# Optimization experiments

Measured on AMD Instinct MI355X. Metric: run time of the kernel, lower is better.

The kernel has to match this reference:

```python
import jax, jax.numpy as jnp
import numpy as np

B = 128
K = 16
# (in_ch, featdim, dim) per stage, matching conv1..conv11
DIMS = [(3, 8, 2048), (8, 32, 1024), (32, 64, 512), (64, 64, 256), (64, 64, 128),
        (64, 128, 64), (128, 256, 32), (256, 512, 16), (512, 512, 8), (512, 512, 4),
        (512, 1024, 2)]


def setup_inputs() -> dict:
    key = jax.random.key(0)
    ks = jax.random.split(key, 64)
    inp = {"x": jax.random.normal(ks[0], (B, 3, 2048), dtype=jnp.float32)}
    i = 1
    for li, (cin, cf, d) in enumerate(DIMS, start=1):
        inp[f"W{li}"] = jax.random.normal(ks[i], (3 * cf, cin), dtype=jnp.float32) / np.sqrt(cin).astype(np.float32); i += 1
        inp[f"b{li}"] = jax.random.normal(ks[i], (3 * cf,), dtype=jnp.float32) * 0.01; i += 1
        inp[f"sel{li}"] = jax.random.randint(ks[i], (d,), 0, 3); i += 1
    inp["fcW"] = jax.random.normal(ks[i], (K, 1024), dtype=jnp.float32) / np.sqrt(1024).astype(np.float32); i += 1
    inp["fcb"] = jax.random.normal(ks[i], (K,), dtype=jnp.float32) * 0.01
    return inp


def kdconv(x, W, b, sel, featdim, dim):
    # 1x1 conv == per-position matmul: x [B, Cin, dim] -> y [B, 3*featdim, dim]
    y = jax.nn.relu(jnp.einsum('oi,bin->bon', W, x) + b[None, :, None])
    y = y.reshape(-1, featdim, 3, dim)
    # kd split-dim gather: pick one of the 3 feature groups per position
    y = jnp.take_along_axis(y, sel[None, None, None, :], axis=2)[:, :, 0, :]  # [B, featdim, dim]
    # pairwise max-pool of sibling leaves
    return y.reshape(-1, featdim, dim // 2, 2).max(axis=-1)  # [B, featdim, dim//2]


def reference(x, sel1, sel2, sel3, sel4, sel5, sel6, sel7, sel8, sel9, sel10, sel11,
              W1, b1, W2, b2, W3, b3, W4, b4, W5, b5, W6, b6, W7, b7, W8, b8,
              W9, b9, W10, b10, W11, b11, fcW, fcb):
    Ws = [W1, W2, W3, W4, W5, W6, W7, W8, W9, W10, W11]
    bs = [b1, b2, b3, b4, b5, b6, b7, b8, b9, b10, b11]
    sels = [sel1, sel2, sel3, sel4, sel5, sel6, sel7, sel8, sel9, sel10, sel11]
    h = x
    for (cin, cf, d), W, b, s in zip(DIMS, Ws, bs, sels):
        h = kdconv(h, W, b, s, cf, d)
    h = h.reshape(-1, 1024)  # [B, 1024]
    return jax.nn.log_softmax(h @ fcW.T + fcb, axis=-1)
```

## Files before the change

kernel.cpp:

```cpp
#include <hip/hip_runtime.h>
#include <math.h>

typedef __attribute__((ext_vector_type(8))) short bf16x8;
typedef __attribute__((ext_vector_type(4))) float f32x4;

__device__ __forceinline__ unsigned short f2bf(float f) {
    unsigned u = __builtin_bit_cast(unsigned, f);
    u += 0x7FFF + ((u >> 16) & 1);
    return (unsigned short)(u >> 16);
}
__device__ __forceinline__ float bf2f(unsigned short h) {
    unsigned u = ((unsigned)h) << 16;
    return __builtin_bit_cast(float, u);
}

struct K1Params {
    const float* x;
    const float* W1; const float* B1; const int* S1;
    const float* W2; const float* B2; const int* S2;
    const float* Wsrc[9];
    unsigned short* Wb;
    unsigned short* X3;
};

__global__ __launch_bounds__(256) void k1_kernel(K1Params P)
{
    const int tid = threadIdx.x;

    if (blockIdx.x >= 128) {
        int gt = (blockIdx.x - 128) * 256 + tid;
        const int we[9] = {6144, 12288, 12288, 24576, 98304, 393216, 786432, 786432, 1572864};
        int off = 0;
#pragma unroll
        for (int li = 0; li < 9; ++li) {
            const float4* src = (const float4*)P.Wsrc[li];
            ushort4* dst = (ushort4*)(P.Wb + off);
            int n4 = we[li] >> 2;
            for (int i = gt; i < n4; i += 32768) {
                float4 w = src[i];
                dst[i] = make_ushort4(f2bf(w.x), f2bf(w.y), f2bf(w.z), f2bf(w.w));
            }
            off += we[li];
        }
        return;
    }

    __shared__ float wl1[72], bl1[24], wl2[768], bl2[96];
    __shared__ unsigned short bufL1[16 * 64 * 8];

    if (tid < 72) wl1[tid] = P.W1[tid];
    if (tid >= 128 && tid < 152) bl1[tid - 128] = P.B1[tid - 128];
    for (int i = tid; i < 768; i += 256) wl2[i] = P.W2[i];
    if (tid < 96) bl2[tid] = P.B2[tid];
    __syncthreads();

    const int npT = blockIdx.x >> 1;
    const int b0  = (blockIdx.x & 1) * 64;

    for (int i = tid; i < 1024; i += 256) {
        int pos_l = i >> 6, bl = i & 63;
        int np1 = npT * 16 + pos_l;
        int b = b0 + bl;
        int s0 = P.S1[2 * np1], s1 = P.S1[2 * np1 + 1];
        const float* xb = P.x + (size_t)b * 6144 + 2 * np1;
        float2 c0 = *(const float2*)(xb);
        float2 c1 = *(const float2*)(xb + 2048);
        float2 c2 = *(const float2*)(xb + 4096);
        unsigned short o[8];
#pragma unroll
        for (int f = 0; f < 8; ++f) {
            int r0 = f * 3 + s0, r1 = f * 3 + s1;
            float z0 = fmaf(wl1[r0*3+2], c2.x, fmaf(wl1[r0*3+1], c1.x, fmaf(wl1[r0*3+0], c0.x, bl1[r0])));
            float z1 = fmaf(wl1[r1*3+2], c2.y, fmaf(wl1[r1*3+1], c1.y, fmaf(wl1[r1*3+0], c0.y, bl1[r1])));
            o[f] = f2bf(fmaxf(fmaxf(z0, z1), 0.f));
        }
        unsigned short* dst = &bufL1[((size_t)pos_l * 64 + bl) * 8];
        *(ushort4*)dst       = make_ushort4(o[0], o[1], o[2], o[3]);
        *(ushort4*)(dst + 4) = make_ushort4(o[4], o[5], o[6], o[7]);
    }
    __syncthreads();

    for (int i = tid; i < 512; i += 256) {
        int np_l = i >> 6, bl = i & 63;
        int np2 = npT * 8 + np_l;
        int s0 = P.S2[2 * np2], s1 = P.S2[2 * np2 + 1];
        const unsigned short* r0 = &bufL1[((size_t)(2 * np_l) * 64 + bl) * 8];
        const unsigned short* r1 = &bufL1[((size_t)(2 * np_l + 1) * 64 + bl) * 8];
        float xa[8], xb[8];
        {
            ushort4 u0 = *(const ushort4*)r0, u1 = *(const ushort4*)(r0 + 4);
            ushort4 v0 = *(const ushort4*)r1, v1 = *(const ushort4*)(r1 + 4);
            xa[0]=bf2f(u0.x); xa[1]=bf2f(u0.y); xa[2]=bf2f(u0.z); xa[3]=bf2f(u0.w);
            xa[4]=bf2f(u1.x); xa[5]=bf2f(u1.y); xa[6]=bf2f(u1.z); xa[7]=bf2f(u1.w);
            xb[0]=bf2f(v0.x); xb[1]=bf2f(v0.y); xb[2]=bf2f(v0.z); xb[3]=bf2f(v0.w);
            xb[4]=bf2f(v1.x); xb[5]=bf2f(v1.y); xb[6]=bf2f(v1.z); xb[7]=bf2f(v1.w);
        }
        unsigned short o[32];
#pragma unroll
        for (int f = 0; f < 32; ++f) {
            const float* w0 = &wl2[(f * 3 + s0) * 8];
            const float* w1 = &wl2[(f * 3 + s1) * 8];
            float z0 = bl2[f * 3 + s0], z1 = bl2[f * 3 + s1];
#pragma unroll
            for (int k = 0; k < 8; ++k) {
                z0 = fmaf(w0[k], xa[k], z0);
                z1 = fmaf(w1[k], xb[k], z1);
            }
            o[f] = f2bf(fmaxf(fmaxf(z0, z1), 0.f));
        }
        unsigned short* dst = P.X3 + ((size_t)np2 * 128 + b0 + bl) * 32;
#pragma unroll
        for (int i2 = 0; i2 < 8; ++i2)
            *(ushort4*)(dst + 4 * i2) = make_ushort4(o[4*i2], o[4*i2+1], o[4*i2+2], o[4*i2+3]);
    }
}

template<int CIN>
__device__ __forceinline__ void mfma_tile(
    const unsigned short* a0, const unsigned short* a1,
    const unsigned short* b0p, const unsigned short* b1p,
    f32x4& acc0, f32x4& acc1)
{
#pragma unroll
    for (int k = 0; k < CIN; k += 32) {
        bf16x8 A0 = __builtin_bit_cast(bf16x8, *(const float4*)(const void*)(a0 + k));
        bf16x8 A1 = __builtin_bit_cast(bf16x8, *(const float4*)(const void*)(a1 + k));
        bf16x8 B0 = __builtin_bit_cast(bf16x8, *(const float4*)(const void*)(b0p + k));
        bf16x8 B1 = __builtin_bit_cast(bf16x8, *(const float4*)(const void*)(b1p + k));
        acc0 = __builtin_amdgcn_mfma_f32_16x16x32_bf16(A0, B0, acc0, 0, 0, 0);
        acc1 = __builtin_amdgcn_mfma_f32_16x16x32_bf16(A1, B1, acc1, 0, 0, 0);
    }
}

__device__ __forceinline__ void epilogue_store(
    unsigned short* dst, const f32x4& acc0, const f32x4& acc1,
    const float* bias, int fbase, int s0, int s1)
{
    unsigned short o[4];
#pragma unroll
    for (int r = 0; r < 4; ++r) {
        float v = fmaxf(fmaxf(acc0[r] + bias[(fbase + r) * 3 + s0],
                              acc1[r] + bias[(fbase + r) * 3 + s1]), 0.f);
        o[r] = f2bf(v);
    }
    *(ushort4*)dst = make_ushort4(o[0], o[1], o[2], o[3]);
}

__global__ __launch_bounds__(256) void stage2_kernel(
    const unsigned short* __restrict__ X3,
    const unsigned short* __restrict__ Wb,
    const float* __restrict__ B3, const int* __restrict__ S3,
    const float* __restrict__ B4, const int* __restrict__ S4,
    const float* __restrict__ B5, const int* __restrict__ S5,
    unsigned short* __restrict__ X6)
{
    constexpr int RPE = 72;
    __shared__ unsigned short L3o[4 * 32 * RPE];
    __shared__ unsigned short L4o[2 * 32 * RPE];

    const int tid  = threadIdx.x;
    const int lane = tid & 63;
    const int wv   = tid >> 6;
    const int c = lane & 15, q = lane >> 4;
    const int n5 = blockIdx.x >> 2;
    const int b0 = (blockIdx.x & 3) * 32;

    const unsigned short* W3b = Wb;
    const unsigned short* W4b = Wb + 6144;
    const unsigned short* W5b = Wb + 18432;

    for (int t = wv; t < 32; t += 4) {
        int bt = t & 1, ft = (t >> 1) & 3, j = t >> 3;
        int np = 4 * n5 + j;
        int s0 = __builtin_amdgcn_readfirstlane(S3[2 * np]);
        int s1 = __builtin_amdgcn_readfirstlane(S3[2 * np + 1]);
        int f0 = ft * 16, bl = bt * 16;
        const unsigned short* a0 = W3b + (size_t)((f0 + c) * 3 + s0) * 32 + q * 8;
        const unsigned short* a1 = W3b + (size_t)((f0 + c) * 3 + s1) * 32 + q * 8;
        const unsigned short* bp0 = X3 + ((size_t)(8 * n5 + 2 * j) * 128 + b0 + bl + c) * 32 + q * 8;
        const unsigned short* bp1 = X3 + ((size_t)(8 * n5 + 2 * j + 1) * 128 + b0 + bl + c) * 32 + q * 8;
        f32x4 acc0 = {0.f,0.f,0.f,0.f}, acc1 = {0.f,0.f,0.f,0.f};
        mfma_tile<32>(a0, a1, bp0, bp1, acc0, acc1);
        epilogue_store(&L3o[((size_t)j * 32 + bl + c) * RPE + f0 + q * 4],
                       acc0, acc1, B3, f0 + q * 4, s0, s1);
    }
    __syncthreads();

    for (int t = wv; t < 16; t += 4) {
        int bt = t & 1, ft = (t >> 1) & 3, j = t >> 3;
        int np = 2 * n5 + j;
        int s0 = __builtin_amdgcn_readfirstlane(S4[2 * np]);
        int s1 = __builtin_amdgcn_readfirstlane(S4[2 * np + 1]);
        int f0 = ft * 16, bl = bt * 16;
        const unsigned short* a0 = W4b + (size_t)((f0 + c) * 3 + s0) * 64 + q * 8;
        const unsigned short* a1 = W4b + (size_t)((f0 + c) * 3 + s1) * 64 + q * 8;
        const unsigned short* bp0 = &L3o[((size_t)(2 * j) * 32 + bl + c) * RPE + q * 8];
        const unsigned short* bp1 = &L3o[((size_t)(2 * j + 1) * 32 + bl + c) * RPE + q * 8];
        f32x4 acc0 = {0.f,0.f,0.f,0.f}, acc1 = {0.f,0.f,0.f,0.f};
        mfma_tile<64>(a0, a1, bp0, bp1, acc0, acc1);
        epilogue_store(&L4o[((size_t)j * 32 + bl + c) * RPE + f0 + q * 4],
                       acc0, acc1, B4, f0 + q * 4, s0, s1);
    }
    __syncthreads();

    for (int t = wv; t < 8; t += 4) {
        int bt = t & 1, ft = t >> 1;
        int s0 = __builtin_amdgcn_readfirstlane(S5[2 * n5]);
        int s1 = __builtin_amdgcn_readfirstlane(S5[2 * n5 + 1]);
        int f0 = ft * 16, bl = bt * 16;
        const unsigned short* a0 = W5b + (size_t)((f0 + c) * 3 + s0) * 64 + q * 8;
        const unsigned short* a1 = W5b + (size_t)((f0 + c) * 3 + s1) * 64 + q * 8;
        const unsigned short* bp0 = &L4o[((size_t)(0) * 32 + bl + c) * RPE + q * 8];
        const unsigned short* bp1 = &L4o[((size_t)(1) * 32 + bl + c) * RPE + q * 8];
        f32x4 acc0 = {0.f,0.f,0.f,0.f}, acc1 = {0.f,0.f,0.f,0.f};
        mfma_tile<64>(a0, a1, bp0, bp1, acc0, acc1);
        epilogue_store(X6 + ((size_t)n5 * 128 + b0 + bl + c) * 64 + f0 + q * 4,
                       acc0, acc1, B5, f0 + q * 4, s0, s1);
    }
}

__global__ __launch_bounds__(512) void stage67_kernel(
    const unsigned short* __restrict__ X6,
    const unsigned short* __restrict__ W6b, const float* __restrict__ B6, const int* __restrict__ S6,
    const unsigned short* __restrict__ W7b, const float* __restrict__ B7, const int* __restrict__ S7,
    unsigned short* __restrict__ X8)
{
    constexpr int RPE = 136;
    __shared__ unsigned short L6o[2 * 16 * RPE];

    const int tid  = threadIdx.x;
    const int lane = tid & 63;
    const int wv   = tid >> 6;
    const int c = lane & 15, q = lane >> 4;
    const int n7 = blockIdx.x >> 3;
    const int b0 = (blockIdx.x & 7) * 16;

    for (int t = wv; t < 16; t += 8) {
        int j = t >> 3, ft = t & 7;
        int np = 2 * n7 + j;
        int s0 = __builtin_amdgcn_readfirstlane(S6[2 * np]);
        int s1 = __builtin_amdgcn_readfirstlane(S6[2 * np + 1]);
        int f0 = ft * 16;
        const unsigned short* a0 = W6b + (size_t)((f0 + c) * 3 + s0) * 64 + q * 8;
        const unsigned short* a1 = W6b + (size_t)((f0 + c) * 3 + s1) * 64 + q * 8;
        const unsigned short* bp0 = X6 + ((size_t)(2 * np) * 128 + b0 + c) * 64 + q * 8;
        const unsigned short* bp1 = X6 + ((size_t)(2 * np + 1) * 128 + b0 + c) * 64 + q * 8;
        f32x4 acc0 = {0.f,0.f,0.f,0.f}, acc1 = {0.f,0.f,0.f,0.f};
        mfma_tile<64>(a0, a1, bp0, bp1, acc0, acc1);
        epilogue_store(&L6o[((size_t)j * 16 + c) * RPE + f0 + q * 4],
                       acc0, acc1, B6, f0 + q * 4, s0, s1);
    }
    __syncthreads();

    {
        int s0 = __builtin_amdgcn_readfirstlane(S7[2 * n7]);
        int s1 = __builtin_amdgcn_readfirstlane(S7[2 * n7 + 1]);
        for (int t = wv; t < 16; t += 8) {
            int f0 = t * 16;
            const unsigned short* a0 = W7b + (size_t)((f0 + c) * 3 + s0) * 128 + q * 8;
            const unsigned short* a1 = W7b + (size_t)((f0 + c) * 3 + s1) * 128 + q * 8;
            const unsigned short* bp0 = &L6o[((size_t)(0) * 16 + c) * RPE + q * 8];
            const unsigned short* bp1 = &L6o[((size_t)(1) * 16 + c) * RPE + q * 8];
            f32x4 acc0 = {0.f,0.f,0.f,0.f}, acc1 = {0.f,0.f,0.f,0.f};
            mfma_tile<128>(a0, a1, bp0, bp1, acc0, acc1);
            epilogue_store(X8 + ((size_t)n7 * 128 + b0 + c) * 256 + f0 + q * 4,
                           acc0, acc1, B7, f0 + q * 4, s0, s1);
        }
    }
}

template<int CIN, int CF, int NP, int MW, int NW>
__global__ __launch_bounds__(256) void mfma_kernel(
    const unsigned short* __restrict__ Xin,
    const unsigned short* __restrict__ Wb,
    const float* __restrict__ bias,
    const int*   __restrict__ sel,
    unsigned short* __restrict__ Xout)
{
    constexpr int FT = CF / (16 * MW);
    constexpr int BT = 128 / (16 * NW);

    const int wid  = threadIdx.x >> 6;
    const int lane = threadIdx.x & 63;
    const int task = blockIdx.x * 4 + wid;
    const int bi = task % BT;
    const int fi = (task / BT) % FT;
    const int n  = task / (BT * FT);

    const int c = lane & 15;
    const int q = lane >> 4;
    const int s0 = __builtin_amdgcn_readfirstlane(sel[2 * n]);
    const int s1 = __builtin_amdgcn_readfirstlane(sel[2 * n + 1]);

    const int f0 = fi * 16 * MW;
    const int b0 = bi * 16 * NW;

    const unsigned short* ap[2][MW];
    const unsigned short* bp[2][NW];
#pragma unroll
    for (int p = 0; p < 2; ++p) {
        int s = p ? s1 : s0;
#pragma unroll
        for (int mi = 0; mi < MW; ++mi)
            ap[p][mi] = Wb + (size_t)((f0 + mi * 16 + c) * 3 + s) * CIN + q * 8;
#pragma unroll
        for (int ni = 0; ni < NW; ++ni)
            bp[p][ni] = Xin + ((size_t)(2 * n + p) * 128 + b0 + ni * 16 + c) * CIN + q * 8;
    }

    f32x4 acc[2][MW][NW];
#pragma unroll
    for (int p = 0; p < 2; ++p)
#pragma unroll
        for (int mi = 0; mi < MW; ++mi)
#pragma unroll
            for (int ni = 0; ni < NW; ++ni)
                acc[p][mi][ni] = (f32x4){0.f, 0.f, 0.f, 0.f};

#pragma unroll 2
    for (int k = 0; k < CIN; k += 32) {
        bf16x8 A[2][MW], B[2][NW];
#pragma unroll
        for (int p = 0; p < 2; ++p) {
#pragma unroll
            for (int mi = 0; mi < MW; ++mi)
                A[p][mi] = __builtin_bit_cast(bf16x8, *(const float4*)(const void*)(ap[p][mi] + k));
#pragma unroll
            for (int ni = 0; ni < NW; ++ni)
                B[p][ni] = __builtin_bit_cast(bf16x8, *(const float4*)(const void*)(bp[p][ni] + k));
        }
#pragma unroll
        for (int p = 0; p < 2; ++p)
#pragma unroll
            for (int mi = 0; mi < MW; ++mi)
#pragma unroll
                for (int ni = 0; ni < NW; ++ni)
                    acc[p][mi][ni] = __builtin_amdgcn_mfma_f32_16x16x32_bf16(
                        A[p][mi], B[p][ni], acc[p][mi][ni], 0, 0, 0);
    }

#pragma unroll
    for (int mi = 0; mi < MW; ++mi) {
        int fbase = f0 + mi * 16 + q * 4;
#pragma unroll
        for (int ni = 0; ni < NW; ++ni) {
            int b = b0 + ni * 16 + c;
            epilogue_store(Xout + ((size_t)n * 128 + b) * CF + fbase,
                           acc[0][mi][ni], acc[1][mi][ni], bias, fbase, s0, s1);
        }
    }
}

__global__ __launch_bounds__(256) void fc_logsoftmax_kernel(
    const unsigned short* __restrict__ h, const float* __restrict__ fcW,
    const float* __restrict__ fcb, float* __restrict__ out)
{
    int b   = blockIdx.x;
    int tid = threadIdx.x;
    int k     = tid & 15;
    int chunk = tid >> 4;

    const float* __restrict__ wk = fcW + (size_t)k * 1024;
    const unsigned short* hb = h + (size_t)b * 1024;

    float partial = 0.0f;
    int j0 = chunk * 64;
#pragma unroll 8
    for (int j = 0; j < 64; ++j)
        partial = fmaf(bf2f(hb[j0 + j]), wk[j0 + j], partial);

    __shared__ float red[16][17];
    red[chunk][k] = partial;
    __syncthreads();

    __shared__ float logits[16];
    if (tid < 16) {
        float s = fcb[tid];
#pragma unroll
        for (int c = 0; c < 16; ++c) s += red[c][tid];
        logits[tid] = s;
    }
    __syncthreads();

    if (tid < 16) {
        float mx = -INFINITY;
#pragma unroll
        for (int kk = 0; kk < 16; ++kk) mx = fmaxf(mx, logits[kk]);
        float se = 0.0f;
#pragma unroll
        for (int kk = 0; kk < 16; ++kk) se += expf(logits[kk] - mx);
        out[b * 16 + tid] = logits[tid] - mx - logf(se);
    }
}

extern "C" void kernel_launch(void* const* d_in, const int* in_sizes, int n_in,
                              void* d_out, int out_size, void* d_ws, size_t ws_size,
                              hipStream_t stream)
{
#define WL(i) (const float*)d_in[1 + 3 * (i)]
#define BL(i) (const float*)d_in[2 + 3 * (i)]
#define SL(i) (const int*)  d_in[3 + 3 * (i)]

    unsigned short* bufA = (unsigned short*)d_ws;
    unsigned short* bufB = bufA + 2u * 1024u * 1024u;
    unsigned short* Wb   = bufB + 2u * 1024u * 1024u;

    const int o6 = 30720, o7 = 55296, o8 = 153600,
              o9 = 546816, o10 = 1333248, o11 = 2119680;

    K1Params P;
    P.x = (const float*)d_in[0];
    P.W1 = WL(0); P.B1 = BL(0); P.S1 = SL(0);
    P.W2 = WL(1); P.B2 = BL(1); P.S2 = SL(1);
    for (int i = 0; i < 9; ++i) P.Wsrc[i] = WL(2 + i);
    P.Wb = Wb; P.X3 = bufA;
    k1_kernel<<<256, 256, 0, stream>>>(P);

    stage2_kernel<<<256, 256, 0, stream>>>(bufA, Wb,
        BL(2), SL(2), BL(3), SL(3), BL(4), SL(4), bufB);

    stage67_kernel<<<128, 512, 0, stream>>>(bufB,
        Wb + o6, BL(5), SL(5), Wb + o7, BL(6), SL(6), bufA);

    mfma_kernel<256, 512, 8, 2, 2><<<128, 256, 0, stream>>>(bufA, Wb + o8,  BL(7),  SL(7),  bufB);
    mfma_kernel<512, 512, 4, 1, 1><<<256, 256, 0, stream>>>(bufB, Wb + o9,  BL(8),  SL(8),  bufA);
    mfma_kernel<512, 512, 2, 1, 1><<<128, 256, 0, stream>>>(bufA, Wb + o10, BL(9),  SL(9),  bufB);
    mfma_kernel<512, 1024, 1, 1, 1><<<128, 256, 0, stream>>>(bufB, Wb + o11, BL(10), SL(10), bufA);

    fc_logsoftmax_kernel<<<128, 256, 0, stream>>>(bufA, (const float*)d_in[34], (const float*)d_in[35], (float*)d_out);

#undef WL
#undef BL
#undef SL
}
```

Baseline: 211.0 us.

## Fuse all stages into one cooperative persistent kernel with grid syncs

Merges the eight separate kernel launches into a single cooperative kernel of 256 blocks that runs each stage as a phase separated by grid-wide barriers. Stage 6/7 is re-split across 256 blocks of 256 threads, and layer 8 uses a narrower wave tile so every phase fits the uniform grid. The aim is to remove per-launch overhead and inter-kernel gaps. The cost is grid.sync barriers, possible lower occupancy from the union of shared memory, and idle waves in phases with fewer tasks. A fallback path launches separate kernels if the cooperative launch fails.

Result: slower. 753.2 us (+257.0%).

```diff
diff --git a/kernel.cpp b/kernel.cpp
--- a/kernel.cpp
+++ b/kernel.cpp
@@ -1,5 +1,8 @@
 #include <hip/hip_runtime.h>
+#include <hip/hip_cooperative_groups.h>
 #include <math.h>
+
+namespace cg = cooperative_groups;
 
 typedef __attribute__((ext_vector_type(8))) short bf16x8;
 typedef __attribute__((ext_vector_type(4))) float f32x4;
@@ -14,16 +17,62 @@
     return __builtin_bit_cast(float, u);
 }
 
-struct K1Params {
+#define O_W3 0
+#define O_W4 6144
+#define O_W5 18432
+#define O_W6 30720
+#define O_W7 55296
+#define O_W8 153600
+#define O_W9 546816
+#define O_W10 1333248
+#define O_W11 2119680
+
+struct MegaParams {
     const float* x;
     const float* W1; const float* B1; const int* S1;
     const float* W2; const float* B2; const int* S2;
     const float* Wsrc[9];
+    const float* Bl[9];
+    const int*   Sl[9];
+    const float* fcW; const float* fcb;
     unsigned short* Wb;
-    unsigned short* X3;
+    unsigned short* bufA;
+    unsigned short* bufB;
+    float* out;
 };
 
-__global__ __launch_bounds__(256) void k1_kernel(K1Params P)
+template<int CIN>
+__device__ __forceinline__ void mfma_tile(
+    const unsigned short* a0, const unsigned short* a1,
+    const unsigned short* b0p, const unsigned short* b1p,
+    f32x4& acc0, f32x4& acc1)
+{
+#pragma unroll
+    for (int k = 0; k < CIN; k += 32) {
+        bf16x8 A0 = __builtin_bit_cast(bf16x8, *(const float4*)(const void*)(a0 + k));
+        bf16x8 A1 = __builtin_bit_cast(bf16x8, *(const float4*)(const void*)(a1 + k));
+        bf16x8 B0 = __builtin_bit_cast(bf16x8, *(const float4*)(const void*)(b0p + k));
+        bf16x8 B1 = __builtin_bit_cast(bf16x8, *(const float4*)(const void*)(b1p + k));
+        acc0 = __builtin_amdgcn_mfma_f32_16x16x32_bf16(A0, B0, acc0, 0, 0, 0);
+        acc1 = __builtin_amdgcn_mfma_f32_16x16x32_bf16(A1, B1, acc1, 0, 0, 0);
+    }
+}
+
+__device__ __forceinline__ void epilogue_store(
+    unsigned short* dst, const f32x4& acc0, const f32x4& acc1,
+    const float* bias, int fbase, int s0, int s1)
+{
+    unsigned short o[4];
+#pragma unroll
+    for (int r = 0; r < 4; ++r) {
+        float v = fmaxf(fmaxf(acc0[r] + bias[(fbase + r) * 3 + s0],
+                              acc1[r] + bias[(fbase + r) * 3 + s1]), 0.f);
+        o[r] = f2bf(v);
+    }
+    *(ushort4*)dst = make_ushort4(o[0], o[1], o[2], o[3]);
+}
+
+__device__ __forceinline__ void phase0(const MegaParams& P)
 {
     const int tid = threadIdx.x;
 
@@ -86,14 +135,14 @@
         int s0 = P.S2[2 * np2], s1 = P.S2[2 * np2 + 1];
         const unsigned short* r0 = &bufL1[((size_t)(2 * np_l) * 64 + bl) * 8];
         const unsigned short* r1 = &bufL1[((size_t)(2 * np_l + 1) * 64 + bl) * 8];
-        float xa[8], xb[8];
+        float xa[8], xb2[8];
         {
             ushort4 u0 = *(const ushort4*)r0, u1 = *(const ushort4*)(r0 + 4);
             ushort4 v0 = *(const ushort4*)r1, v1 = *(const ushort4*)(r1 + 4);
             xa[0]=bf2f(u0.x); xa[1]=bf2f(u0.y); xa[2]=bf2f(u0.z); xa[3]=bf2f(u0.w);
             xa[4]=bf2f(u1.x); xa[5]=bf2f(u1.y); xa[6]=bf2f(u1.z); xa[7]=bf2f(u1.w);
-            xb[0]=bf2f(v0.x); xb[1]=bf2f(v0.y); xb[2]=bf2f(v0.z); xb[3]=bf2f(v0.w);
-            xb[4]=bf2f(v1.x); xb[5]=bf2f(v1.y); xb[6]=bf2f(v1.z); xb[7]=bf2f(v1.w);
+            xb2[0]=bf2f(v0.x); xb2[1]=bf2f(v0.y); xb2[2]=bf2f(v0.z); xb2[3]=bf2f(v0.w);
+            xb2[4]=bf2f(v1.x); xb2[5]=bf2f(v1.y); xb2[6]=bf2f(v1.z); xb2[7]=bf2f(v1.w);
         }
         unsigned short o[32];
 #pragma unroll
@@ -104,55 +153,18 @@
 #pragma unroll
             for (int k = 0; k < 8; ++k) {
                 z0 = fmaf(w0[k], xa[k], z0);
-                z1 = fmaf(w1[k], xb[k], z1);
+                z1 = fmaf(w1[k], xb2[k], z1);
             }
             o[f] = f2bf(fmaxf(fmaxf(z0, z1), 0.f));
         }
-        unsigned short* dst = P.X3 + ((size_t)np2 * 128 + b0 + bl) * 32;
+        unsigned short* dst = P.bufA + ((size_t)np2 * 128 + b0 + bl) * 32;
 #pragma unroll
         for (int i2 = 0; i2 < 8; ++i2)
             *(ushort4*)(dst + 4 * i2) = make_ushort4(o[4*i2], o[4*i2+1], o[4*i2+2], o[4*i2+3]);
     }
 }
 
-template<int CIN>
-__device__ __forceinline__ void mfma_tile(
-    const unsigned short* a0, const unsigned short* a1,
-    const unsigned short* b0p, const unsigned short* b1p,
-    f32x4& acc0, f32x4& acc1)
-{
-#pragma unroll
-    for (int k = 0; k < CIN; k += 32) {
-        bf16x8 A0 = __builtin_bit_cast(bf16x8, *(const float4*)(const void*)(a0 + k));
-        bf16x8 A1 = __builtin_bit_cast(bf16x8, *(const float4*)(const void*)(a1 + k));
-        bf16x8 B0 = __builtin_bit_cast(bf16x8, *(const float4*)(const void*)(b0p + k));
-        bf16x8 B1 = __builtin_bit_cast(bf16x8, *(const float4*)(const void*)(b1p + k));
-        acc0 = __builtin_amdgcn_mfma_f32_16x16x32_bf16(A0, B0, acc0, 0, 0, 0);
-        acc1 = __builtin_amdgcn_mfma_f32_16x16x32_bf16(A1, B1, acc1, 0, 0, 0);
-    }
-}
-
-__device__ __forceinline__ void epilogue_store(
-    unsigned short* dst, const f32x4& acc0, const f32x4& acc1,
-    const float* bias, int fbase, int s0, int s1)
-{
-    unsigned short o[4];
-#pragma unroll
-    for (int r = 0; r < 4; ++r) {
-        float v = fmaxf(fmaxf(acc0[r] + bias[(fbase + r) * 3 + s0],
-                              acc1[r] + bias[(fbase + r) * 3 + s1]), 0.f);
-        o[r] = f2bf(v);
-    }
-    *(ushort4*)dst = make_ushort4(o[0], o[1], o[2], o[3]);
-}
-
-__global__ __launch_bounds__(256) void stage2_kernel(
-    const unsigned short* __restrict__ X3,
-    const unsigned short* __restrict__ Wb,
-    const float* __restrict__ B3, const int* __restrict__ S3,
-    const float* __restrict__ B4, const int* __restrict__ S4,
-    const float* __restrict__ B5, const int* __restrict__ S5,
-    unsigned short* __restrict__ X6)
+__device__ __forceinline__ void phase1(const MegaParams& P)
 {
     constexpr int RPE = 72;
     __shared__ unsigned short L3o[4 * 32 * RPE];
@@ -165,9 +177,14 @@
     const int n5 = blockIdx.x >> 2;
     const int b0 = (blockIdx.x & 3) * 32;
 
-    const unsigned short* W3b = Wb;
-    const unsigned short* W4b = Wb + 6144;
-    const unsigned short* W5b = Wb + 18432;
+    const unsigned short* X3  = P.bufA;
+    unsigned short*       X6  = P.bufB;
+    const unsigned short* W3b = P.Wb + O_W3;
+    const unsigned short* W4b = P.Wb + O_W4;
+    const unsigned short* W5b = P.Wb + O_W5;
+    const float* B3 = P.Bl[0]; const int* S3 = P.Sl[0];
+    const float* B4 = P.Bl[1]; const int* S4 = P.Sl[1];
+    const float* B5 = P.Bl[2]; const int* S5 = P.Sl[2];
 
     for (int t = wv; t < 32; t += 4) {
         int bt = t & 1, ft = (t >> 1) & 3, j = t >> 3;
@@ -219,11 +236,7 @@
     }
 }
 
-__global__ __launch_bounds__(512) void stage67_kernel(
-    const unsigned short* __restrict__ X6,
-    const unsigned short* __restrict__ W6b, const float* __restrict__ B6, const int* __restrict__ S6,
-    const unsigned short* __restrict__ W7b, const float* __restrict__ B7, const int* __restrict__ S7,
-    unsigned short* __restrict__ X8)
+__device__ __forceinline__ void phase2(const MegaParams& P)
 {
     constexpr int RPE = 136;
     __shared__ unsigned short L6o[2 * 16 * RPE];
@@ -232,10 +245,19 @@
     const int lane = tid & 63;
     const int wv   = tid >> 6;
     const int c = lane & 15, q = lane >> 4;
-    const int n7 = blockIdx.x >> 3;
-    const int b0 = (blockIdx.x & 7) * 16;
-
-    for (int t = wv; t < 16; t += 8) {
+    const int n7   = blockIdx.x >> 4;
+    const int sub  = blockIdx.x & 15;
+    const int b0   = (sub & 7) * 16;
+    const int half = sub >> 3;
+
+    const unsigned short* X6  = P.bufB;
+    unsigned short*       X8  = P.bufA;
+    const unsigned short* W6b = P.Wb + O_W6;
+    const unsigned short* W7b = P.Wb + O_W7;
+    const float* B6 = P.Bl[3]; const int* S6 = P.Sl[3];
+    const float* B7 = P.Bl[4]; const int* S7 = P.Sl[4];
+
+    for (int t = wv; t < 16; t += 4) {
         int j = t >> 3, ft = t & 7;
         int np = 2 * n7 + j;
         int s0 = __builtin_amdgcn_readfirstlane(S6[2 * np]);
@@ -255,8 +277,8 @@
     {
         int s0 = __builtin_amdgcn_readfirstlane(S7[2 * n7]);
         int s1 = __builtin_amdgcn_readfirstlane(S7[2 * n7 + 1]);
-        for (int t = wv; t < 16; t += 8) {
-            int f0 = t * 16;
+        for (int t = wv; t < 8; t += 4) {
+            int f0 = (half * 8 + t) * 16;
             const unsigned short* a0 = W7b + (size_t)((f0 + c) * 3 + s0) * 128 + q * 8;
             const unsigned short* a1 = W7b + (size_t)((f0 + c) * 3 + s1) * 128 + q * 8;
             const unsigned short* bp0 = &L6o[((size_t)(0) * 16 + c) * RPE + q * 8];
@@ -270,7 +292,8 @@
 }
 
 template<int CIN, int CF, int NP, int MW, int NW>
-__global__ __launch_bounds__(256) void mfma_kernel(
+__device__ __forceinline__ void mfma_layer(
+    int gwave, int lane,
     const unsigned short* __restrict__ Xin,
     const unsigned short* __restrict__ Wb,
     const float* __restrict__ bias,
@@ -279,10 +302,10 @@
 {
     constexpr int FT = CF / (16 * MW);
     constexpr int BT = 128 / (16 * NW);
-
-    const int wid  = threadIdx.x >> 6;
-    const int lane = threadIdx.x & 63;
-    const int task = blockIdx.x * 4 + wid;
+    constexpr int NT = NP * FT * BT;
+    if (gwave >= NT) return;
+
+    const int task = gwave;
     const int bi = task % BT;
     const int fi = (task / BT) % FT;
     const int n  = task / (BT * FT);
@@ -351,17 +374,19 @@
     }
 }
 
-__global__ __launch_bounds__(256) void fc_logsoftmax_kernel(
-    const unsigned short* __restrict__ h, const float* __restrict__ fcW,
-    const float* __restrict__ fcb, float* __restrict__ out)
-{
+__device__ __forceinline__ void phase_fc(const MegaParams& P)
+{
+    if (blockIdx.x >= 128) return;
+    __shared__ float red[16][17];
+    __shared__ float logits[16];
+
     int b   = blockIdx.x;
     int tid = threadIdx.x;
     int k     = tid & 15;
     int chunk = tid >> 4;
 
-    const float* __restrict__ wk = fcW + (size_t)k * 1024;
-    const unsigned short* hb = h + (size_t)b * 1024;
+    const float* __restrict__ wk = P.fcW + (size_t)k * 1024;
+    const unsigned short* hb = P.bufA + (size_t)b * 1024;
 
     float partial = 0.0f;
     int j0 = chunk * 64;
@@ -369,13 +394,11 @@
     for (int j = 0; j < 64; ++j)
         partial = fmaf(bf2f(hb[j0 + j]), wk[j0 + j], partial);
 
-    __shared__ float red[16][17];
     red[chunk][k] = partial;
     __syncthreads();
 
-    __shared__ float logits[16];
     if (tid < 16) {
-        float s = fcb[tid];
+        float s = P.fcb[tid];
 #pragma unroll
         for (int c = 0; c < 16; ++c) s += red[c][tid];
         logits[tid] = s;
@@ -389,47 +412,83 @@
         float se = 0.0f;
 #pragma unroll
         for (int kk = 0; kk < 16; ++kk) se += expf(logits[kk] - mx);
-        out[b * 16 + tid] = logits[tid] - mx - logf(se);
-    }
+        P.out[b * 16 + tid] = logits[tid] - mx - logf(se);
+    }
+}
+
+__global__ __launch_bounds__(256) void meganet(MegaParams P)
+{
+    cg::grid_group grid = cg::this_grid();
+    const int gwave = blockIdx.x * 4 + (threadIdx.x >> 6);
+    const int lane  = threadIdx.x & 63;
+
+    phase0(P);
+    __threadfence(); grid.sync(); __threadfence();
+    phase1(P);
+    __threadfence(); grid.sync(); __threadfence();
+    phase2(P);
+    __threadfence(); grid.sync(); __threadfence();
+    mfma_layer<256, 512, 8, 2, 1>(gwave, lane, P.bufA, P.Wb + O_W8,  P.Bl[5], P.Sl[5], P.bufB);
+    __threadfence(); grid.sync(); __threadfence();
+    mfma_layer<512, 512, 4, 1, 1>(gwave, lane, P.bufB, P.Wb + O_W9,  P.Bl[6], P.Sl[6], P.bufA);
+    __threadfence(); grid.sync(); __threadfence();
+    mfma_layer<512, 512, 2, 1, 1>(gwave, lane, P.bufA, P.Wb + O_W10, P.Bl[7], P.Sl[7], P.bufB);
+    __threadfence(); grid.sync(); __threadfence();
+    mfma_layer<512, 1024, 1, 1, 1>(gwave, lane, P.bufB, P.Wb + O_W11, P.Bl[8], P.Sl[8], P.bufA);
+    __threadfence(); grid.sync(); __threadfence();
+    phase_fc(P);
+}
+
+__global__ __launch_bounds__(256) void k_phase0(MegaParams P) { phase0(P); }
+__global__ __launch_bounds__(256) void k_phase1(MegaParams P) { phase1(P); }
+__global__ __launch_bounds__(256) void k_phase2(MegaParams P) { phase2(P); }
+__global__ __launch_bounds__(256) void k_fc(MegaParams P)     { phase_fc(P); }
+
+template<int CIN, int CF, int NP, int MW, int NW>
+__global__ __launch_bounds__(256) void k_mfma(
+    const unsigned short* __restrict__ Xin,
+    const unsigned short* __restrict__ Wb,
+    const float* __restrict__ bias,
+    const int*   __restrict__ sel,
+    unsigned short* __restrict__ Xout)
+{
+    mfma_layer<CIN, CF, NP, MW, NW>(blockIdx.x * 4 + (threadIdx.x >> 6),
+                                    threadIdx.x & 63, Xin, Wb, bias, sel, Xout);
 }
 
 extern "C" void kernel_launch(void* const* d_in, const int* in_sizes, int n_in,
                               void* d_out, int out_size, void* d_ws, size_t ws_size,
                               hipStream_t stream)
 {
-#define WL(i) (const float*)d_in[1 + 3 * (i)]
-#define BL(i) (const float*)d_in[2 + 3 * (i)]
-#define SL(i) (const int*)  d_in[3 + 3 * (i)]
+    MegaParams P;
+    P.x  = (const float*)d_in[0];
+    P.W1 = (const float*)d_in[1]; P.B1 = (const float*)d_in[2]; P.S1 = (const int*)d_in[3];
+    P.W2 = (const float*)d_in[4]; P.B2 = (const float*)d_in[5]; P.S2 = (const int*)d_in[6];
+    for (int i = 0; i < 9; ++i) {
+        P.Wsrc[i] = (const float*)d_in[7 + 3 * i];
+        P.Bl[i]   = (const float*)d_in[8 + 3 * i];
+        P.Sl[i]   = (const int*)  d_in[9 + 3 * i];
+    }
+    P.fcW = (const float*)d_in[34];
+    P.fcb = (const float*)d_in[35];
 
     unsigned short* bufA = (unsigned short*)d_ws;
-    unsigned short* bufB = bufA + 2u * 1024u * 1024u;
-    unsigned short* Wb   = bufB + 2u * 1024u * 1024u;
-
-    const int o6 = 30720, o7 = 55296, o8 = 153600,
-              o9 = 546816, o10 = 1333248, o11 = 2119680;
-
-    K1Params P;
-    P.x = (const float*)d_in[0];
-    P.W1 = WL(0); P.B1 = BL(0); P.S1 = SL(0);
-    P.W2 = WL(1); P.B2 = BL(1); P.S2 = SL(1);
-    for (int i = 0; i < 9; ++i) P.Wsrc[i] = WL(2 + i);
-    P.Wb = Wb; P.X3 = bufA;
-    k1_kernel<<<256, 256, 0, stream>>>(P);
-
-    stage2_kernel<<<256, 256, 0, stream>>>(bufA, Wb,
-        BL(2), SL(2), BL(3), SL(3), BL(4), SL(4), bufB);
-
-    stage67_kernel<<<128, 512, 0, stream>>>(bufB,
-        Wb + o6, BL(5), SL(5), Wb + o7, BL(6), SL(6), bufA);
-
-    mfma_kernel<256, 512, 8, 2, 2><<<128, 256, 0, stream>>>(bufA, Wb + o8,  BL(7),  SL(7),  bufB);
-    mfma_kernel<512, 512, 4, 1, 1><<<256, 256, 0, stream>>>(bufB, Wb + o9,  BL(8),  SL(8),  bufA);
-    mfma_kernel<512, 512, 2, 1, 1><<<128, 256, 0, stream>>>(bufA, Wb + o10, BL(9),  SL(9),  bufB);
-    mfma_kernel<512, 1024, 1, 1, 1><<<128, 256, 0, stream>>>(bufB, Wb + o11, BL(10), SL(10), bufA);
-
-    fc_logsoftmax_kernel<<<128, 256, 0, stream>>>(bufA, (const float*)d_in[34], (const float*)d_in[35], (float*)d_out);
-
-#undef WL
-#undef BL
-#undef SL
-}
+    P.bufA = bufA;
+    P.bufB = bufA + 2u * 1024u * 1024u;
+    P.Wb   = P.bufB + 2u * 1024u * 1024u;
+    P.out  = (float*)d_out;
+
+    void* args[] = { (void*)&P };
+    hipError_t err = hipLaunchCooperativeKernel(meganet, dim3(256), dim3(256),
+                                                (void**)args, 0u, stream);
+    if (err != hipSuccess) {
+        k_phase0<<<256, 256, 0, stream>>>(P);
+        k_phase1<<<256, 256, 0, stream>>>(P);
+        k_phase2<<<256, 256, 0, stream>>>(P);
+        k_mfma<256, 512, 8, 2, 1><<<256, 256, 0, stream>>>(P.bufA, P.Wb + O_W8,  P.Bl[5], P.Sl[5], P.bufB);
+        k_mfma<512, 512, 4, 1, 1><<<256, 256, 0, stream>>>(P.bufB, P.Wb + O_W9,  P.Bl[6], P.Sl[6], P.bufA);
+        k_mfma<512, 512, 2, 1, 1><<<128, 256, 0, stream>>>(P.bufA, P.Wb + O_W10, P.Bl[7], P.Sl[7], P.bufB);
+        k_mfma<512, 1024, 1, 1, 1><<<128, 256, 0, stream>>>(P.bufB, P.Wb + O_W11, P.Bl[8], P.Sl[8], P.bufA);
+        k_fc<<<128, 256, 0, stream>>>(P);
+    }
+}
```
